# Kernel tuning notes

Hardware: AMD Instinct MI355X
Metric: run time of the kernel (lower is better)

Reference implementation:

```python
import jax, jax.numpy as jnp
import numpy as np

N_NODES = 100000
N_EDGES = 1200000
N_GRAPHS = 256
IN_C, HID_C, OUT_C = 5, 64, 2


def gcn_conv(x, src, dst, W, b, n_nodes):
    """PyG GCNConv: h = x@W; add self-loops; deg from target col (edge weight 1);
    norm = deg^{-1/2}[src]*deg^{-1/2}[dst]; scatter-add messages into dst; + bias."""
    loop = jnp.arange(n_nodes, dtype=src.dtype)
    s = jnp.concatenate([src, loop])
    d = jnp.concatenate([dst, loop])
    deg = jax.ops.segment_sum(jnp.ones_like(d, dtype=x.dtype), d, num_segments=n_nodes)
    dinv = jnp.where(deg > 0, jax.lax.rsqrt(deg), 0.0)
    norm = dinv[s] * dinv[d]                     # [E+N]
    h = x @ W                                    # [N, out]
    msg = h[s] * norm[:, None]                   # gather + scale  [E+N, out]
    out = jax.ops.segment_sum(msg, d, num_segments=n_nodes)  # scatter-add
    return out + b


def setup_inputs() -> dict:
    key = jax.random.key(0)
    ks = jax.random.split(key, 10)
    x = jax.random.normal(ks[0], (N_NODES, IN_C), dtype=jnp.float32)
    edge_index = jax.random.randint(ks[1], (2, N_EDGES), 0, N_NODES, dtype=jnp.int64)
    batch = jnp.sort(jax.random.randint(ks[2], (N_NODES,), 0, N_GRAPHS, dtype=jnp.int64))
    def glorot(k, fan_in, fan_out):
        lim = np.sqrt(6.0 / (fan_in + fan_out))
        return jax.random.uniform(k, (fan_in, fan_out), jnp.float32, -lim, lim)
    W1 = glorot(ks[3], IN_C, HID_C)
    b1 = jnp.zeros((HID_C,), jnp.float32)
    W2 = glorot(ks[4], HID_C, HID_C)
    b2 = jnp.zeros((HID_C,), jnp.float32)
    Wfc = glorot(ks[5], HID_C, OUT_C)
    bfc = jnp.zeros((OUT_C,), jnp.float32)
    return {"x": x, "edge_index": edge_index, "batch": batch,
            "W1": W1, "b1": b1, "W2": W2, "b2": b2, "Wfc": Wfc, "bfc": bfc}


def reference(x, edge_index, batch, W1, b1, W2, b2, Wfc, bfc):
    src, dst = edge_index[0], edge_index[1]
    h = jax.nn.relu(gcn_conv(x, src, dst, W1, b1, N_NODES))
    h = jax.nn.relu(gcn_conv(h, src, dst, W2, b2, N_NODES))
    # global_mean_pool over graph ids in `batch`
    sums = jax.ops.segment_sum(h, batch, num_segments=N_GRAPHS)          # [G, H]
    cnts = jax.ops.segment_sum(jnp.ones((h.shape[0],), h.dtype), batch,
                               num_segments=N_GRAPHS)                    # [G]
    pooled = sums / jnp.maximum(cnts, 1.0)[:, None]
    return pooled @ Wfc + bfc                                            # [G, 2]
```

## Files before the change

### kernel.cpp

```cpp
#include <hip/hip_runtime.h>

#define N_NODES 100000
#define N_EDGES 1200000
#define N_GRAPHS 256
#define IN_C 5
#define HID_C 64
#define OUT_C 2

#define BSH 7
#define BNODES 128
#define NB ((N_NODES + BNODES - 1) / BNODES)
#define CAPB 2048
#define EPB 2048
#define NBLK_E ((N_EDGES + EPB - 1) / EPB)
#define GNPW 8
#define G1NPW 4

typedef unsigned int uint32;

__device__ __forceinline__ uint32 f2bf(float f) {
    uint32 x = __float_as_uint(f);
    return (x + 0x7FFFu + ((x >> 16) & 1u)) >> 16;
}
__device__ __forceinline__ float bflo(uint32 r) { return __uint_as_float(r << 16); }
__device__ __forceinline__ float bfhi(uint32 r) { return __uint_as_float(r & 0xFFFF0000u); }

__global__ void k_bscatter(const int* __restrict__ src, const int* __restrict__ dst,
                           int* __restrict__ bcnt, int* __restrict__ pairs,
                           float* __restrict__ pooled) {
    __shared__ int h[NB];
    if (blockIdx.x < (N_GRAPHS * HID_C) / 256)
        pooled[blockIdx.x * 256 + threadIdx.x] = 0.f;
    for (int i = threadIdx.x; i < NB; i += blockDim.x) h[i] = 0;
    __syncthreads();
    int e0 = blockIdx.x * EPB;
    int e1 = e0 + EPB; if (e1 > N_EDGES) e1 = N_EDGES;
    for (int e = e0 + threadIdx.x; e < e1; e += blockDim.x)
        atomicAdd(&h[dst[e] >> BSH], 1);
    __syncthreads();
    for (int i = threadIdx.x; i < NB; i += blockDim.x)
        if (h[i]) h[i] = (i << 11) + atomicAdd(&bcnt[i], h[i]);
    __syncthreads();
    for (int e = e0 + threadIdx.x; e < e1; e += blockDim.x) {
        int d = dst[e];
        int pos = atomicAdd(&h[d >> BSH], 1);
        pairs[pos] = ((d & (BNODES - 1)) << 17) | src[e];
    }
}

__global__ void k_bsort_g1(const int* __restrict__ pairs, const int* __restrict__ bcnt,
                           const float* __restrict__ x, const float* __restrict__ W1,
                           int* __restrict__ csr, int* __restrict__ rs,
                           int* __restrict__ cnt, float* __restrict__ dinv,
                           uint32* __restrict__ g) {
    __shared__ int hist[BNODES];
    __shared__ int tmp[BNODES];
    __shared__ int cur[BNODES];
    __shared__ float sdv[BNODES];
    __shared__ __align__(16) float sW1[IN_C * HID_C];
    __shared__ float sx[BNODES * IN_C];
    int b = blockIdx.x;
    int t = threadIdx.x;
    int base = b << BSH;
    if (t < BNODES) hist[t] = 0;
    for (int i = t; i < IN_C * HID_C; i += 256) sW1[i] = W1[i];
    for (int i = t; i < BNODES * IN_C; i += 256) {
        int gi = base * IN_C + i;
        sx[i] = (gi < N_NODES * IN_C) ? x[gi] : 0.f;
    }
    __syncthreads();
    int s = b << 11;
    int n = bcnt[b];
    for (int i = t; i < n; i += 256)
        atomicAdd(&hist[pairs[s + i] >> 17], 1);
    __syncthreads();
    int v = (t < BNODES) ? hist[t] : 0;
    if (t < BNODES) tmp[t] = v;
    __syncthreads();
    for (int off = 1; off < BNODES; off <<= 1) {
        int a = (t < BNODES && t >= off) ? tmp[t - off] : 0;
        __syncthreads();
        if (t < BNODES) tmp[t] += a;
        __syncthreads();
    }
    float dv_t = rsqrtf((float)v + 1.0f);
    if (t < BNODES) {
        cur[t] = tmp[t] - v;
        sdv[t] = dv_t;
        if (base + t < N_NODES) {
            rs[base + t] = s + tmp[t] - v;
            cnt[base + t] = v;
            dinv[base + t] = dv_t;
        }
    }
    __syncthreads();
    for (int i = t; i < n; i += 256) {
        int p = pairs[s + i];
        int pos = atomicAdd(&cur[p >> 17], 1);
        csr[s + pos] = p & 0x1FFFF;
    }
    for (int idx = t; idx < BNODES * 32; idx += 256) {
        int nl = idx >> 5, c2 = idx & 31;
        int node = base + nl;
        if (node >= N_NODES) break;
        float s0 = 0.f, s1 = 0.f;
#pragma unroll
        for (int k = 0; k < IN_C; ++k) {
            float xv = sx[nl * IN_C + k];
            float2 wv = *(const float2*)&sW1[k * HID_C + 2 * c2];
            s0 += xv * wv.x;
            s1 += xv * wv.y;
        }
        float dv = sdv[nl];
        g[(unsigned)node * 32 + c2] = (f2bf(s1 * dv) << 16) | f2bf(s0 * dv);
    }
}

__global__ void __launch_bounds__(256) k_gather_g2(
        const uint32* __restrict__ g1t, const int* __restrict__ csr,
        const int* __restrict__ rs, const int* __restrict__ cnt,
        const float* __restrict__ dinv, const float* __restrict__ b1,
        const float* __restrict__ W2, uint32* __restrict__ g2t) {
    __shared__ __align__(16) float sW2[HID_C * HID_C];
    __shared__ float srow[4][HID_C];
    int tid = threadIdx.x;
    for (int i = tid; i < HID_C * HID_C; i += 256) sW2[i] = W2[i];
    __syncthreads();
    int w = tid >> 6;
    int wv = __builtin_amdgcn_readfirstlane(blockIdx.x * 4 + w);
    int n0 = wv * G1NPW;
    if (n0 >= N_NODES) return;
    int n1 = n0 + G1NPW; if (n1 > N_NODES) n1 = N_NODES;
    int lane = tid & 63;
    int half = lane >> 5;
    int c2 = lane & 31;
    float bias0 = b1[2 * c2], bias1 = b1[2 * c2 + 1];
    for (int v = n0; v < n1; ++v) {
        int k0 = rs[v];
        int n = cnt[v];
        float s0 = 0.f, s1 = 0.f;
        if (half == 0) {
            uint32 r = g1t[(unsigned)v * 32 + c2];
            s0 = bflo(r); s1 = bfhi(r);
        }
        int i = 0;
        for (; i + 7 < n; i += 8) {
            int u0 = csr[k0 + i + 0], u1 = csr[k0 + i + 1];
            int u2 = csr[k0 + i + 2], u3 = csr[k0 + i + 3];
            int u4 = csr[k0 + i + 4], u5 = csr[k0 + i + 5];
            int u6 = csr[k0 + i + 6], u7 = csr[k0 + i + 7];
            int a0 = half ? u1 : u0;
            int a1 = half ? u3 : u2;
            int a2 = half ? u5 : u4;
            int a3 = half ? u7 : u6;
            uint32 r0 = g1t[(unsigned)a0 * 32 + c2];
            uint32 r1 = g1t[(unsigned)a1 * 32 + c2];
            uint32 r2 = g1t[(unsigned)a2 * 32 + c2];
            uint32 r3 = g1t[(unsigned)a3 * 32 + c2];
            s0 += (bflo(r0) + bflo(r1)) + (bflo(r2) + bflo(r3));
            s1 += (bfhi(r0) + bfhi(r1)) + (bfhi(r2) + bfhi(r3));
        }
        for (; i + 1 < n; i += 2) {
            int u0 = csr[k0 + i], u1 = csr[k0 + i + 1];
            int a = half ? u1 : u0;
            uint32 r = g1t[(unsigned)a * 32 + c2];
            s0 += bflo(r); s1 += bfhi(r);
        }
        if (i < n && half == 0) {
            uint32 r = g1t[(unsigned)csr[k0 + i] * 32 + c2];
            s0 += bflo(r); s1 += bfhi(r);
        }
        s0 += __shfl_xor(s0, 32);
        s1 += __shfl_xor(s1, 32);
        float dv = dinv[v];
        float o0 = fmaxf(s0 * dv + bias0, 0.f);
        float o1 = fmaxf(s1 * dv + bias1, 0.f);
        if (half == 0) *(float2*)&srow[w][2 * c2] = make_float2(o0, o1);
        int kb = half << 5;
        float a0 = 0.f, a1 = 0.f;
#pragma unroll 8
        for (int j = 0; j < 32; ++j) {
            float hv = srow[w][kb + j];
            float2 wvv = *(const float2*)&sW2[(kb + j) * HID_C + 2 * c2];
            a0 += hv * wvv.x;
            a1 += hv * wvv.y;
        }
        a0 += __shfl_xor(a0, 32);
        a1 += __shfl_xor(a1, 32);
        if (half == 0)
            g2t[(unsigned)v * 32 + c2] = (f2bf(a1 * dv) << 16) | f2bf(a0 * dv);
    }
}

__global__ void k_gather2p(const uint32* __restrict__ g, const int* __restrict__ csr,
                           const int* __restrict__ rs, const int* __restrict__ cnt,
                           const float* __restrict__ dinv, const float* __restrict__ b,
                           const int* __restrict__ batch, float* __restrict__ pooled) {
    int wv = __builtin_amdgcn_readfirstlane(
        blockIdx.x * (blockDim.x >> 6) + (threadIdx.x >> 6));
    int n0 = wv * GNPW;
    if (n0 >= N_NODES) return;
    int n1 = n0 + GNPW; if (n1 > N_NODES) n1 = N_NODES;
    int lane = threadIdx.x & 63;
    int half = lane >> 5;
    int c2 = lane & 31;
    float bias0 = b[2 * c2], bias1 = b[2 * c2 + 1];
    float p0 = 0.f, p1 = 0.f;
    int curg = batch[n0];
    for (int v = n0; v < n1; ++v) {
        int k0 = rs[v];
        int n = cnt[v];
        float s0 = 0.f, s1 = 0.f;
        if (half == 0) {
            uint32 r = g[(unsigned)v * 32 + c2];
            s0 = bflo(r); s1 = bfhi(r);
        }
        int i = 0;
        for (; i + 7 < n; i += 8) {
            int u0 = csr[k0 + i + 0], u1 = csr[k0 + i + 1];
            int u2 = csr[k0 + i + 2], u3 = csr[k0 + i + 3];
            int u4 = csr[k0 + i + 4], u5 = csr[k0 + i + 5];
            int u6 = csr[k0 + i + 6], u7 = csr[k0 + i + 7];
            int a0 = half ? u1 : u0;
            int a1 = half ? u3 : u2;
            int a2 = half ? u5 : u4;
            int a3 = half ? u7 : u6;
            uint32 r0 = g[(unsigned)a0 * 32 + c2];
            uint32 r1 = g[(unsigned)a1 * 32 + c2];
            uint32 r2 = g[(unsigned)a2 * 32 + c2];
            uint32 r3 = g[(unsigned)a3 * 32 + c2];
            s0 += (bflo(r0) + bflo(r1)) + (bflo(r2) + bflo(r3));
            s1 += (bfhi(r0) + bfhi(r1)) + (bfhi(r2) + bfhi(r3));
        }
        for (; i + 1 < n; i += 2) {
            int u0 = csr[k0 + i], u1 = csr[k0 + i + 1];
            int a = half ? u1 : u0;
            uint32 r = g[(unsigned)a * 32 + c2];
            s0 += bflo(r); s1 += bfhi(r);
        }
        if (i < n && half == 0) {
            uint32 r = g[(unsigned)csr[k0 + i] * 32 + c2];
            s0 += bflo(r); s1 += bfhi(r);
        }
        s0 += __shfl_xor(s0, 32);
        s1 += __shfl_xor(s1, 32);
        float dv = dinv[v];
        float o0 = fmaxf(s0 * dv + bias0, 0.f);
        float o1 = fmaxf(s1 * dv + bias1, 0.f);
        int gg = batch[v];
        if (gg != curg) {
            if (half == 0) {
                atomicAdd(&pooled[curg * HID_C + 2 * c2], p0);
                atomicAdd(&pooled[curg * HID_C + 2 * c2 + 1], p1);
            }
            p0 = 0.f; p1 = 0.f; curg = gg;
        }
        p0 += o0; p1 += o1;
    }
    if (half == 0) {
        atomicAdd(&pooled[curg * HID_C + 2 * c2], p0);
        atomicAdd(&pooled[curg * HID_C + 2 * c2 + 1], p1);
    }
}

__global__ void k_fc(const float* __restrict__ pooled, const int* __restrict__ batch,
                     const float* __restrict__ Wfc, const float* __restrict__ bfc,
                     float* __restrict__ out) {
    int g = blockIdx.x;
    int c = threadIdx.x;
    int lo = 0, hi = N_NODES;
    while (lo < hi) { int mid = (lo + hi) >> 1; if (batch[mid] < g) lo = mid + 1; else hi = mid; }
    int start = lo;
    hi = N_NODES;
    while (lo < hi) { int mid = (lo + hi) >> 1; if (batch[mid] < g + 1) lo = mid + 1; else hi = mid; }
    int n = lo - start;
    float pv = pooled[g * HID_C + c] / (float)(n > 0 ? n : 1);
    float o0 = pv * Wfc[c * OUT_C + 0];
    float o1 = pv * Wfc[c * OUT_C + 1];
#pragma unroll
    for (int off = 32; off > 0; off >>= 1) {
        o0 += __shfl_down(o0, off);
        o1 += __shfl_down(o1, off);
    }
    if (c == 0) {
        out[g * OUT_C + 0] = o0 + bfc[0];
        out[g * OUT_C + 1] = o1 + bfc[1];
    }
}

extern "C" void kernel_launch(void* const* d_in, const int* in_sizes, int n_in,
                              void* d_out, int out_size, void* d_ws, size_t ws_size,
                              hipStream_t stream) {
    const float* x    = (const float*)d_in[0];
    const int*   ei   = (const int*)d_in[1];
    const int*   src  = ei;
    const int*   dst  = ei + N_EDGES;
    const int*   batch= (const int*)d_in[2];
    const float* W1   = (const float*)d_in[3];
    const float* b1   = (const float*)d_in[4];
    const float* W2   = (const float*)d_in[5];
    const float* b2   = (const float*)d_in[6];
    const float* Wfc  = (const float*)d_in[7];
    const float* bfc  = (const float*)d_in[8];
    float* out = (float*)d_out;

    float*  ws     = (float*)d_ws;
    int*    bcnt   = (int*)ws;
    float*  pooled = ws + 1024;
    float*  dinv   = pooled + 16384;
    int*    cnt    = (int*)(dinv + 100352);
    int*    rs     = cnt + 100352;
    int*    pairs  = rs + 100352;
    int*    csr    = pairs + (NB * CAPB);
    uint32* g1tab  = (uint32*)(csr + (NB * CAPB));
    uint32* g2tab  = g1tab + N_NODES * 32;

    hipMemsetAsync(bcnt, 0, 1024 * sizeof(int), stream);

    k_bscatter<<<NBLK_E, 256, 0, stream>>>(src, dst, bcnt, pairs, pooled);
    k_bsort_g1<<<NB, 256, 0, stream>>>(pairs, bcnt, x, W1, csr, rs, cnt, dinv, g1tab);

    {
        int waves = (N_NODES + G1NPW - 1) / G1NPW;
        int blocks = (waves + 3) / 4;
        k_gather_g2<<<blocks, 256, 0, stream>>>(g1tab, csr, rs, cnt, dinv, b1, W2, g2tab);
    }

    {
        int waves = (N_NODES + GNPW - 1) / GNPW;
        int blocks = (waves + 3) / 4;
        k_gather2p<<<blocks, 256, 0, stream>>>(g2tab, csr, rs, cnt, dinv, b2, batch, pooled);
    }

    k_fc<<<N_GRAPHS, 64, 0, stream>>>(pooled, batch, Wfc, bfc, out);
}
```

Measured before the change: 221.7 us.

## Aggregate raw 5-dim features before W1 and process two nodes per wave in layer 2

Layer 1 now gathers the dinv-scaled 5-channel input features (padded to 8 floats) over neighbors and applies W1 afterwards, instead of gathering precomputed 64-channel bf16 rows. This relies on linearity to shrink the per-edge gather from 128 bytes to about 20 bytes. The second gather kernel assigns one node to each half-wave rather than splitting a node's edges across halves, which removes the cross-half shuffle reduction but can leave lanes idle when degrees differ. Layer-1 aggregation is now done in fp32 rather than bf16.

```diff
diff --git a/kernel.cpp b/kernel.cpp
--- a/kernel.cpp
+++ b/kernel.cpp
@@ -14,7 +14,7 @@
 #define EPB 2048
 #define NBLK_E ((N_EDGES + EPB - 1) / EPB)
 #define GNPW 8
-#define G1NPW 4
+#define L1NPW 8
 
 typedef unsigned int uint32;
 
@@ -48,26 +48,19 @@
     }
 }
 
-__global__ void k_bsort_g1(const int* __restrict__ pairs, const int* __restrict__ bcnt,
-                           const float* __restrict__ x, const float* __restrict__ W1,
+__global__ void k_bsort_xs(const int* __restrict__ pairs, const int* __restrict__ bcnt,
+                           const float* __restrict__ x,
                            int* __restrict__ csr, int* __restrict__ rs,
                            int* __restrict__ cnt, float* __restrict__ dinv,
-                           uint32* __restrict__ g) {
+                           float* __restrict__ xs) {
     __shared__ int hist[BNODES];
     __shared__ int tmp[BNODES];
     __shared__ int cur[BNODES];
     __shared__ float sdv[BNODES];
-    __shared__ __align__(16) float sW1[IN_C * HID_C];
-    __shared__ float sx[BNODES * IN_C];
     int b = blockIdx.x;
     int t = threadIdx.x;
     int base = b << BSH;
     if (t < BNODES) hist[t] = 0;
-    for (int i = t; i < IN_C * HID_C; i += 256) sW1[i] = W1[i];
-    for (int i = t; i < BNODES * IN_C; i += 256) {
-        int gi = base * IN_C + i;
-        sx[i] = (gi < N_NODES * IN_C) ? x[gi] : 0.f;
-    }
     __syncthreads();
     int s = b << 11;
     int n = bcnt[b];
@@ -99,103 +92,103 @@
         int pos = atomicAdd(&cur[p >> 17], 1);
         csr[s + pos] = p & 0x1FFFF;
     }
-    for (int idx = t; idx < BNODES * 32; idx += 256) {
-        int nl = idx >> 5, c2 = idx & 31;
+    for (int i = t; i < BNODES * 8; i += 256) {
+        int nl = i >> 3, k = i & 7;
         int node = base + nl;
-        if (node >= N_NODES) break;
-        float s0 = 0.f, s1 = 0.f;
-#pragma unroll
-        for (int k = 0; k < IN_C; ++k) {
-            float xv = sx[nl * IN_C + k];
-            float2 wv = *(const float2*)&sW1[k * HID_C + 2 * c2];
-            s0 += xv * wv.x;
-            s1 += xv * wv.y;
-        }
-        float dv = sdv[nl];
-        g[(unsigned)node * 32 + c2] = (f2bf(s1 * dv) << 16) | f2bf(s0 * dv);
-    }
-}
-
-__global__ void __launch_bounds__(256) k_gather_g2(
-        const uint32* __restrict__ g1t, const int* __restrict__ csr,
+        if (node < N_NODES && k < IN_C)
+            xs[(unsigned)node * 8 + k] = x[(unsigned)node * IN_C + k] * sdv[nl];
+    }
+}
+
+__global__ void __launch_bounds__(256) k_l1(
+        const float* __restrict__ xs, const int* __restrict__ csr,
         const int* __restrict__ rs, const int* __restrict__ cnt,
         const float* __restrict__ dinv, const float* __restrict__ b1,
-        const float* __restrict__ W2, uint32* __restrict__ g2t) {
+        const float* __restrict__ W1, const float* __restrict__ W2,
+        uint32* __restrict__ g2t) {
     __shared__ __align__(16) float sW2[HID_C * HID_C];
-    __shared__ float srow[4][HID_C];
+    __shared__ __align__(16) float sW1[IN_C * HID_C];
+    __shared__ float sagg[4][L1NPW][8];
+    __shared__ float srow[4][2][HID_C];
     int tid = threadIdx.x;
     for (int i = tid; i < HID_C * HID_C; i += 256) sW2[i] = W2[i];
+    for (int i = tid; i < IN_C * HID_C; i += 256) sW1[i] = W1[i];
     __syncthreads();
     int w = tid >> 6;
-    int wv = __builtin_amdgcn_readfirstlane(blockIdx.x * 4 + w);
-    int n0 = wv * G1NPW;
-    if (n0 >= N_NODES) return;
-    int n1 = n0 + G1NPW; if (n1 > N_NODES) n1 = N_NODES;
     int lane = tid & 63;
-    int half = lane >> 5;
-    int c2 = lane & 31;
-    float bias0 = b1[2 * c2], bias1 = b1[2 * c2 + 1];
-    for (int v = n0; v < n1; ++v) {
+    int base = (blockIdx.x * 4 + w) * L1NPW;
+
+    int g = lane >> 3, l = lane & 7;
+    int v = base + g;
+    float a0 = 0.f, a1 = 0.f, a2 = 0.f, a3 = 0.f, a4 = 0.f;
+    if (v < N_NODES) {
         int k0 = rs[v];
         int n = cnt[v];
-        float s0 = 0.f, s1 = 0.f;
-        if (half == 0) {
-            uint32 r = g1t[(unsigned)v * 32 + c2];
-            s0 = bflo(r); s1 = bfhi(r);
-        }
-        int i = 0;
-        for (; i + 7 < n; i += 8) {
-            int u0 = csr[k0 + i + 0], u1 = csr[k0 + i + 1];
-            int u2 = csr[k0 + i + 2], u3 = csr[k0 + i + 3];
-            int u4 = csr[k0 + i + 4], u5 = csr[k0 + i + 5];
-            int u6 = csr[k0 + i + 6], u7 = csr[k0 + i + 7];
-            int a0 = half ? u1 : u0;
-            int a1 = half ? u3 : u2;
-            int a2 = half ? u5 : u4;
-            int a3 = half ? u7 : u6;
-            uint32 r0 = g1t[(unsigned)a0 * 32 + c2];
-            uint32 r1 = g1t[(unsigned)a1 * 32 + c2];
-            uint32 r2 = g1t[(unsigned)a2 * 32 + c2];
-            uint32 r3 = g1t[(unsigned)a3 * 32 + c2];
-            s0 += (bflo(r0) + bflo(r1)) + (bflo(r2) + bflo(r3));
-            s1 += (bfhi(r0) + bfhi(r1)) + (bfhi(r2) + bfhi(r3));
-        }
-        for (; i + 1 < n; i += 2) {
-            int u0 = csr[k0 + i], u1 = csr[k0 + i + 1];
-            int a = half ? u1 : u0;
-            uint32 r = g1t[(unsigned)a * 32 + c2];
-            s0 += bflo(r); s1 += bfhi(r);
-        }
-        if (i < n && half == 0) {
-            uint32 r = g1t[(unsigned)csr[k0 + i] * 32 + c2];
-            s0 += bflo(r); s1 += bfhi(r);
-        }
-        s0 += __shfl_xor(s0, 32);
-        s1 += __shfl_xor(s1, 32);
-        float dv = dinv[v];
-        float o0 = fmaxf(s0 * dv + bias0, 0.f);
-        float o1 = fmaxf(s1 * dv + bias1, 0.f);
-        if (half == 0) *(float2*)&srow[w][2 * c2] = make_float2(o0, o1);
+        if (l == 0) {
+            float4 p = *(const float4*)&xs[(unsigned)v * 8];
+            a0 = p.x; a1 = p.y; a2 = p.z; a3 = p.w;
+            a4 = xs[(unsigned)v * 8 + 4];
+        }
+        for (int i = l; i < n; i += 8) {
+            int u = csr[k0 + i];
+            float4 p = *(const float4*)&xs[(unsigned)u * 8];
+            float p4 = xs[(unsigned)u * 8 + 4];
+            a0 += p.x; a1 += p.y; a2 += p.z; a3 += p.w; a4 += p4;
+        }
+    }
+#pragma unroll
+    for (int off = 4; off; off >>= 1) {
+        a0 += __shfl_xor(a0, off);
+        a1 += __shfl_xor(a1, off);
+        a2 += __shfl_xor(a2, off);
+        a3 += __shfl_xor(a3, off);
+        a4 += __shfl_xor(a4, off);
+    }
+    if (l == 0 && v < N_NODES) {
+        sagg[w][g][0] = a0; sagg[w][g][1] = a1; sagg[w][g][2] = a2;
+        sagg[w][g][3] = a3; sagg[w][g][4] = a4;
+    }
+
+    int half = lane >> 5, c2 = lane & 31;
+    float bias0 = b1[2 * c2], bias1 = b1[2 * c2 + 1];
+    for (int gg = 0; gg < L1NPW; ++gg) {
+        int node = base + gg;
+        if (node >= N_NODES) break;
+        float dv = dinv[node];
+        float q0 = sagg[w][gg][0], q1 = sagg[w][gg][1], q2 = sagg[w][gg][2],
+              q3 = sagg[w][gg][3], q4 = sagg[w][gg][4];
+        float2 w0 = *(const float2*)&sW1[0 * HID_C + 2 * c2];
+        float2 w1v = *(const float2*)&sW1[1 * HID_C + 2 * c2];
+        float2 w2v = *(const float2*)&sW1[2 * HID_C + 2 * c2];
+        float2 w3v = *(const float2*)&sW1[3 * HID_C + 2 * c2];
+        float2 w4v = *(const float2*)&sW1[4 * HID_C + 2 * c2];
+        float s0 = q0 * w0.x + q1 * w1v.x + q2 * w2v.x + q3 * w3v.x + q4 * w4v.x;
+        float s1 = q0 * w0.y + q1 * w1v.y + q2 * w2v.y + q3 * w3v.y + q4 * w4v.y;
+        float h0 = fmaxf(s0 * dv + bias0, 0.f);
+        float h1 = fmaxf(s1 * dv + bias1, 0.f);
+        int buf = gg & 1;
+        if (half == 0) *(float2*)&srow[w][buf][2 * c2] = make_float2(h0, h1);
         int kb = half << 5;
-        float a0 = 0.f, a1 = 0.f;
+        float t0 = 0.f, t1 = 0.f;
 #pragma unroll 8
         for (int j = 0; j < 32; ++j) {
-            float hv = srow[w][kb + j];
+            float hv = srow[w][buf][kb + j];
             float2 wvv = *(const float2*)&sW2[(kb + j) * HID_C + 2 * c2];
-            a0 += hv * wvv.x;
-            a1 += hv * wvv.y;
-        }
-        a0 += __shfl_xor(a0, 32);
-        a1 += __shfl_xor(a1, 32);
+            t0 += hv * wvv.x;
+            t1 += hv * wvv.y;
+        }
+        t0 += __shfl_xor(t0, 32);
+        t1 += __shfl_xor(t1, 32);
         if (half == 0)
-            g2t[(unsigned)v * 32 + c2] = (f2bf(a1 * dv) << 16) | f2bf(a0 * dv);
-    }
-}
-
-__global__ void k_gather2p(const uint32* __restrict__ g, const int* __restrict__ csr,
-                           const int* __restrict__ rs, const int* __restrict__ cnt,
-                           const float* __restrict__ dinv, const float* __restrict__ b,
-                           const int* __restrict__ batch, float* __restrict__ pooled) {
+            g2t[(unsigned)node * 32 + c2] = (f2bf(t1 * dv) << 16) | f2bf(t0 * dv);
+    }
+}
+
+__global__ void __launch_bounds__(256) k_gather2p(
+        const uint32* __restrict__ g, const int* __restrict__ csr,
+        const int* __restrict__ rs, const int* __restrict__ cnt,
+        const float* __restrict__ dinv, const float* __restrict__ b,
+        const int* __restrict__ batch, float* __restrict__ pooled) {
     int wv = __builtin_amdgcn_readfirstlane(
         blockIdx.x * (blockDim.x >> 6) + (threadIdx.x >> 6));
     int n0 = wv * GNPW;
@@ -206,12 +199,15 @@
     int c2 = lane & 31;
     float bias0 = b[2 * c2], bias1 = b[2 * c2 + 1];
     float p0 = 0.f, p1 = 0.f;
-    int curg = batch[n0];
-    for (int v = n0; v < n1; ++v) {
-        int k0 = rs[v];
-        int n = cnt[v];
+    int curg = -1;
+    for (int vb = n0; vb < n1; vb += 2) {
+        int v = vb + half;
+        int valid = (v < n1);
+        int k0 = 0, n = 0;
         float s0 = 0.f, s1 = 0.f;
-        if (half == 0) {
+        if (valid) {
+            k0 = rs[v];
+            n = cnt[v];
             uint32 r = g[(unsigned)v * 32 + c2];
             s0 = bflo(r); s1 = bfhi(r);
         }
@@ -221,43 +217,49 @@
             int u2 = csr[k0 + i + 2], u3 = csr[k0 + i + 3];
             int u4 = csr[k0 + i + 4], u5 = csr[k0 + i + 5];
             int u6 = csr[k0 + i + 6], u7 = csr[k0 + i + 7];
-            int a0 = half ? u1 : u0;
-            int a1 = half ? u3 : u2;
-            int a2 = half ? u5 : u4;
-            int a3 = half ? u7 : u6;
-            uint32 r0 = g[(unsigned)a0 * 32 + c2];
-            uint32 r1 = g[(unsigned)a1 * 32 + c2];
-            uint32 r2 = g[(unsigned)a2 * 32 + c2];
-            uint32 r3 = g[(unsigned)a3 * 32 + c2];
+            uint32 r0 = g[(unsigned)u0 * 32 + c2];
+            uint32 r1 = g[(unsigned)u1 * 32 + c2];
+            uint32 r2 = g[(unsigned)u2 * 32 + c2];
+            uint32 r3 = g[(unsigned)u3 * 32 + c2];
+            uint32 r4 = g[(unsigned)u4 * 32 + c2];
+            uint32 r5 = g[(unsigned)u5 * 32 + c2];
+            uint32 r6 = g[(unsigned)u6 * 32 + c2];
+            uint32 r7 = g[(unsigned)u7 * 32 + c2];
+            s0 += ((bflo(r0) + bflo(r1)) + (bflo(r2) + bflo(r3)))
+                + ((bflo(r4) + bflo(r5)) + (bflo(r6) + bflo(r7)));
+            s1 += ((bfhi(r0) + bfhi(r1)) + (bfhi(r2) + bfhi(r3)))
+                + ((bfhi(r4) + bfhi(r5)) + (bfhi(r6) + bfhi(r7)));
+        }
+        for (; i + 3 < n; i += 4) {
+            int u0 = csr[k0 + i + 0], u1 = csr[k0 + i + 1];
+            int u2 = csr[k0 + i + 2], u3 = csr[k0 + i + 3];
+            uint32 r0 = g[(unsigned)u0 * 32 + c2];
+            uint32 r1 = g[(unsigned)u1 * 32 + c2];
+            uint32 r2 = g[(unsigned)u2 * 32 + c2];
+            uint32 r3 = g[(unsigned)u3 * 32 + c2];
             s0 += (bflo(r0) + bflo(r1)) + (bflo(r2) + bflo(r3));
             s1 += (bfhi(r0) + bfhi(r1)) + (bfhi(r2) + bfhi(r3));
         }
-        for (; i + 1 < n; i += 2) {
-            int u0 = csr[k0 + i], u1 = csr[k0 + i + 1];
-            int a = half ? u1 : u0;
-            uint32 r = g[(unsigned)a * 32 + c2];
-            s0 += bflo(r); s1 += bfhi(r);
-        }
-        if (i < n && half == 0) {
+        for (; i < n; ++i) {
             uint32 r = g[(unsigned)csr[k0 + i] * 32 + c2];
             s0 += bflo(r); s1 += bfhi(r);
         }
-        s0 += __shfl_xor(s0, 32);
-        s1 += __shfl_xor(s1, 32);
-        float dv = dinv[v];
-        float o0 = fmaxf(s0 * dv + bias0, 0.f);
-        float o1 = fmaxf(s1 * dv + bias1, 0.f);
-        int gg = batch[v];
-        if (gg != curg) {
-            if (half == 0) {
-                atomicAdd(&pooled[curg * HID_C + 2 * c2], p0);
-                atomicAdd(&pooled[curg * HID_C + 2 * c2 + 1], p1);
+        if (valid) {
+            float dv = dinv[v];
+            float o0 = fmaxf(s0 * dv + bias0, 0.f);
+            float o1 = fmaxf(s1 * dv + bias1, 0.f);
+            int gg = batch[v];
+            if (gg != curg) {
+                if (curg >= 0) {
+                    atomicAdd(&pooled[curg * HID_C + 2 * c2], p0);
+                    atomicAdd(&pooled[curg * HID_C + 2 * c2 + 1], p1);
+                }
+                p0 = 0.f; p1 = 0.f; curg = gg;
             }
-            p0 = 0.f; p1 = 0.f; curg = gg;
-        }
-        p0 += o0; p1 += o1;
-    }
-    if (half == 0) {
+            p0 += o0; p1 += o1;
+        }
+    }
+    if (curg >= 0) {
         atomicAdd(&pooled[curg * HID_C + 2 * c2], p0);
         atomicAdd(&pooled[curg * HID_C + 2 * c2 + 1], p1);
     }
@@ -312,18 +314,17 @@
     int*    rs     = cnt + 100352;
     int*    pairs  = rs + 100352;
     int*    csr    = pairs + (NB * CAPB);
-    uint32* g1tab  = (uint32*)(csr + (NB * CAPB));
-    uint32* g2tab  = g1tab + N_NODES * 32;
+    float*  xs     = (float*)(csr + (NB * CAPB));
+    uint32* g2tab  = (uint32*)(xs + N_NODES * 8);
 
     hipMemsetAsync(bcnt, 0, 1024 * sizeof(int), stream);
 
     k_bscatter<<<NBLK_E, 256, 0, stream>>>(src, dst, bcnt, pairs, pooled);
-    k_bsort_g1<<<NB, 256, 0, stream>>>(pairs, bcnt, x, W1, csr, rs, cnt, dinv, g1tab);
+    k_bsort_xs<<<NB, 256, 0, stream>>>(pairs, bcnt, x, csr, rs, cnt, dinv, xs);
 
     {
-        int waves = (N_NODES + G1NPW - 1) / G1NPW;
-        int blocks = (waves + 3) / 4;
-        k_gather_g2<<<blocks, 256, 0, stream>>>(g1tab, csr, rs, cnt, dinv, b1, W2, g2tab);
+        int blocks = (N_NODES + 4 * L1NPW - 1) / (4 * L1NPW);
+        k_l1<<<blocks, 256, 0, stream>>>(xs, csr, rs, cnt, dinv, b1, W1, W2, g2tab);
     }
 
     {
```

Result: slower. 228.0 us (+2.8%).
